# Kernel optimization log

Measured on AMD Instinct MI355X. Metric: run time of the kernel, lower is better.

Reference implementation:

```python
import jax, jax.numpy as jnp
import numpy as np

N = 100000
E = 3200000
D = 512

def setup_inputs() -> dict:
    key = jax.random.key(0)
    ks = jax.random.split(key, 6)
    X = jax.random.normal(ks[0], (N, D), dtype=jnp.float32)
    edge_row = jax.random.randint(ks[1], (E,), 0, N, dtype=jnp.int32)
    edge_col = jax.random.randint(ks[2], (E,), 0, N, dtype=jnp.int32)
    edge_val = jax.random.uniform(ks[3], (E,), dtype=jnp.float32)
    # glorot-uniform-ish init for weights
    lim = (6.0 / (D + D)) ** 0.5
    W1 = jax.random.uniform(ks[4], (D, D), dtype=jnp.float32, minval=-lim, maxval=lim)
    W2 = jax.random.uniform(ks[5], (D, D), dtype=jnp.float32, minval=-lim, maxval=lim)
    return {"X": X, "edge_row": edge_row, "edge_col": edge_col,
            "edge_val": edge_val, "W1": W1, "W2": W2}

def _spmm(edge_row, edge_col, edge_val, H):
    # out[r] = sum_{e: row[e]==r} val[e] * H[col[e]]
    msgs = edge_val[:, None] * H[edge_col]          # [E, D]
    return jax.ops.segment_sum(msgs, edge_row, num_segments=N)

def reference(X, edge_row, edge_col, edge_val, W1, W2):
    # layer 1: An @ (X @ W1), tanh activation, no bias
    h = jnp.tanh(_spmm(edge_row, edge_col, edge_val, X @ W1))
    # layer 2
    h = jnp.tanh(_spmm(edge_row, edge_col, edge_val, h @ W2))
    # tf.nn.l2_normalize(curr, axis=1)
    norm = jnp.sqrt(jnp.maximum(jnp.sum(h * h, axis=1, keepdims=True), 1e-12))
    return h / norm
```

## Files before the change

kernel.cpp:

```cpp
#include <hip/hip_runtime.h>
#include <hip/hip_fp16.h>

#define D_DIM 512

typedef __attribute__((ext_vector_type(8))) _Float16 half8;
typedef __attribute__((ext_vector_type(4))) float f32x4;
typedef __attribute__((ext_vector_type(2))) float float2v;

__device__ inline unsigned short f16b(float f) {
  return __half_as_ushort(__float2half(f));
}


__device__ inline void glds16(const _Float16* g, _Float16* l) {
  __builtin_amdgcn_global_load_lds(
      (const __attribute__((address_space(1))) void*)g,
      (__attribute__((address_space(3))) void*)l, 16, 0, 0);
}


__global__ __launch_bounds__(256) void k_hist(const int* __restrict__ row, int* __restrict__ cnt, int E) {
  int i = blockIdx.x * blockDim.x + threadIdx.x;
  if (i < E) atomicAdd(&cnt[row[i]], 1);
}

__global__ __launch_bounds__(1024) void k_scanA(const int* __restrict__ cnt, int* __restrict__ rp,
                                                int* __restrict__ bsum, int n) {
  __shared__ int s[1024];
  int i = blockIdx.x * 1024 + threadIdx.x;
  int v = (i < n) ? cnt[i] : 0;
  s[threadIdx.x] = v;
  __syncthreads();
  for (int off = 1; off < 1024; off <<= 1) {
    int t = (threadIdx.x >= off) ? s[threadIdx.x - off] : 0;
    __syncthreads();
    s[threadIdx.x] += t;
    __syncthreads();
  }
  if (i < n) rp[i] = s[threadIdx.x] - v;
  if (threadIdx.x == 1023) bsum[blockIdx.x] = s[1023];
}

__global__ __launch_bounds__(1024) void k_scanB(int* __restrict__ bsum, int nb) {
  __shared__ int s[1024];
  int v = (threadIdx.x < nb) ? bsum[threadIdx.x] : 0;
  s[threadIdx.x] = v;
  __syncthreads();
  for (int off = 1; off < 1024; off <<= 1) {
    int t = (threadIdx.x >= off) ? s[threadIdx.x - off] : 0;
    __syncthreads();
    s[threadIdx.x] += t;
    __syncthreads();
  }
  if (threadIdx.x < nb) bsum[threadIdx.x] = s[threadIdx.x] - v;
}

__global__ __launch_bounds__(256) void k_scanC(int* __restrict__ rp, const int* __restrict__ bsum, int n, int E) {
  int i = blockIdx.x * 256 + threadIdx.x;
  if (i < n) rp[i] += bsum[i >> 10];
  if (i == 0) rp[n] = E;
}

__global__ __launch_bounds__(256) void k_scatter(const int* __restrict__ row, const int* __restrict__ col,
                                                 const float* __restrict__ val, int* __restrict__ cur,
                                                 int2* __restrict__ edat, int E) {
  int i = blockIdx.x * blockDim.x + threadIdx.x;
  if (i < E) {
    int r = row[i];
    int p = atomicAdd(&cur[r], 1);
    edat[p] = make_int2(col[i], __float_as_int(val[i]));
  }
}


__global__ __launch_bounds__(256) void k_convA(const float* __restrict__ X, unsigned* __restrict__ Xf,
                                               long nValid4, long nTot4) {
  long i = (long)blockIdx.x * 256 + threadIdx.x;
  long stride = (long)gridDim.x * 256;
  for (; i < nTot4; i += stride) {
    float4 x = make_float4(0.f, 0.f, 0.f, 0.f);
    if (i < nValid4) x = ((const float4*)X)[i];
    uint2 v;
    v.x = (unsigned)f16b(x.x) | ((unsigned)f16b(x.y) << 16);
    v.y = (unsigned)f16b(x.z) | ((unsigned)f16b(x.w) << 16);
    const long r = i >> 7;
    const int c0 = (int)(i & 127) * 4;
    const long halfidx = ((r >> 4) * 16 + (c0 >> 5)) * 512 + ((c0 >> 3) & 3) * 128 + (r & 15) * 8 + (c0 & 7);
    ((uint2*)Xf)[halfidx >> 2] = v;
  }
}


__global__ __launch_bounds__(256) void k_repackW(const float* __restrict__ W, _Float16* __restrict__ Wf) {
  int n = blockIdx.x * 256 + threadIdx.x;
  int kg = blockIdx.y;
  half8 v;
#pragma unroll
  for (int j = 0; j < 8; ++j) v[j] = (_Float16)W[(kg * 8 + j) * D_DIM + n];
  const long halfidx = ((long)(kg >> 2) * 32 + (n >> 4)) * 512 + (kg & 3) * 128 + (n & 15) * 8;
  *(half8*)(Wf + halfidx) = v;
}


__global__ __launch_bounds__(256) void k_gemm(const _Float16* __restrict__ A,
                                              const _Float16* __restrict__ B,
                                              _Float16* __restrict__ Cout, int MB) {
  const int id = blockIdx.x;
  const int xcd = id & 7;
  const int sgrid = id >> 3;
  const int panel = (sgrid >> 2) * 8 + xcd;
  if (panel >= MB) return;
  const int nb = sgrid & 3;

  const int tid = threadIdx.x;
  const int lane = tid & 63;
  const int w = tid >> 6;
  const int wr = w >> 1, wc = w & 1;
  const int c = lane & 15, g = lane >> 4;
  const long r0 = (long)panel * 128 + wr * 64;
  const int n0 = nb * 128 + wc * 64;

  __shared__ __align__(16) char smem[32768];
  _Float16* Asl = (_Float16*)smem;
  _Float16* Bsl = (_Float16*)(smem + 16384);

  f32x4 acc[4][4] = {};

  const int f0 = w, f1 = w + 4;
  const long aF0 = ((long)(panel * 8 + f0) * 16) * 512 + lane * 8;
  const long aF1 = ((long)(panel * 8 + f1) * 16) * 512 + lane * 8;
  const long bBase = ((long)nb * 8) * 512 + lane * 8;

  for (int s = 0; s < 8; ++s) {
    const int k5a = 2 * s, k5b = 2 * s + 1;
    glds16(A + aF0 + (long)k5a * 512, Asl + (0 * 8 + f0) * 512);
    glds16(A + aF0 + (long)k5b * 512, Asl + (1 * 8 + f0) * 512);
    glds16(A + aF1 + (long)k5a * 512, Asl + (0 * 8 + f1) * 512);
    glds16(A + aF1 + (long)k5b * 512, Asl + (1 * 8 + f1) * 512);
    glds16(B + bBase + ((long)k5a * 32 + f0) * 512, Bsl + (0 * 8 + f0) * 512);
    glds16(B + bBase + ((long)k5b * 32 + f0) * 512, Bsl + (1 * 8 + f0) * 512);
    glds16(B + bBase + ((long)k5a * 32 + f1) * 512, Bsl + (0 * 8 + f1) * 512);
    glds16(B + bBase + ((long)k5b * 32 + f1) * 512, Bsl + (1 * 8 + f1) * 512);
    __syncthreads();
#pragma unroll
    for (int k5loc = 0; k5loc < 2; ++k5loc) {
      half8 a[4], b[4];
#pragma unroll
      for (int mi = 0; mi < 4; ++mi)
        a[mi] = *(const half8*)(Asl + (k5loc * 8 + wr * 4 + mi) * 512 + lane * 8);
#pragma unroll
      for (int ni = 0; ni < 4; ++ni)
        b[ni] = *(const half8*)(Bsl + (k5loc * 8 + wc * 4 + ni) * 512 + lane * 8);
#pragma unroll
      for (int mi = 0; mi < 4; ++mi)
#pragma unroll
        for (int ni = 0; ni < 4; ++ni)
          acc[mi][ni] = __builtin_amdgcn_mfma_f32_16x16x32_f16(a[mi], b[ni], acc[mi][ni], 0, 0, 0);
    }
    __syncthreads();
  }

  float (*ep)[16][68] = (float (*)[16][68])smem;
#pragma unroll
  for (int m = 0; m < 4; ++m) {
#pragma unroll
    for (int nf = 0; nf < 4; ++nf)
#pragma unroll
      for (int j = 0; j < 4; ++j)
        ep[w][g * 4 + j][nf * 16 + c] = acc[m][nf][j];
    __syncthreads();
    {
      const int row = lane >> 2;
      const int ch = lane & 3;
      float v[16];
#pragma unroll
      for (int q = 0; q < 16; ++q) v[q] = ep[w][row][ch * 16 + q];
      half8 h0, h1;
#pragma unroll
      for (int q = 0; q < 8; ++q) {
        h0[q] = (_Float16)v[q];
        h1[q] = (_Float16)v[8 + q];
      }
      _Float16* dst = Cout + (r0 + m * 16 + row) * D_DIM + n0 + ch * 16;
      *(half8*)dst = h0;
      *(half8*)(dst + 8) = h1;
    }
    __syncthreads();
  }
}


template <int MODE>
__global__ __launch_bounds__(256) void k_spmm(const unsigned short* __restrict__ T, const int* __restrict__ rp,
                                              const int2* __restrict__ edat,
                                              unsigned* __restrict__ Hf, float* __restrict__ out) {
  __shared__ float p[4][D_DIM];
  __shared__ float wss[4];
  const int r = blockIdx.x;
  const int tid = threadIdx.x;
  const int w = tid >> 6, lane = tid & 63;
  const int beg = rp[r], end = rp[r + 1];
  const int cnt = end - beg;
  const int eb = beg + ((cnt * w) >> 2);
  const int ee = beg + ((cnt * (w + 1)) >> 2);

  float acc[8] = {};
  const uint4* Tv = (const uint4*)T;
  for (int e = eb; e < ee; ++e) {
    const int2 ed = edat[e];
    const float v = __int_as_float(ed.y);
    uint4 x = Tv[(long)ed.x * 64 + lane];
    unsigned xs[4] = {x.x, x.y, x.z, x.w};
#pragma unroll
    for (int q = 0; q < 4; ++q) {
      float2 f = __half22float2(__builtin_bit_cast(__half2, xs[q]));
      acc[2 * q] = fmaf(v, f.x, acc[2 * q]);
      acc[2 * q + 1] = fmaf(v, f.y, acc[2 * q + 1]);
    }
  }
  *(float4*)&p[w][lane * 8] = make_float4(acc[0], acc[1], acc[2], acc[3]);
  *(float4*)&p[w][lane * 8 + 4] = make_float4(acc[4], acc[5], acc[6], acc[7]);
  __syncthreads();

  const int c = tid * 2;
  float s0 = p[0][c] + p[1][c] + p[2][c] + p[3][c];
  float s1 = p[0][c + 1] + p[1][c + 1] + p[2][c + 1] + p[3][c + 1];
  s0 = tanhf(s0);
  s1 = tanhf(s1);

  if (MODE == 0) {
    unsigned hv = (unsigned)f16b(s0) | ((unsigned)f16b(s1) << 16);
    const long halfidx = ((long)(r >> 4) * 16 + (c >> 5)) * 512 + ((c >> 3) & 3) * 128 + (r & 15) * 8 + (c & 7);
    __builtin_nontemporal_store(hv, Hf + (halfidx >> 1));
  } else {
    float ss = fmaf(s0, s0, s1 * s1);
#pragma unroll
    for (int off = 1; off < 64; off <<= 1) ss += __shfl_xor(ss, off);
    if (lane == 0) wss[w] = ss;
    __syncthreads();
    const float tot = wss[0] + wss[1] + wss[2] + wss[3];
    const float sc = rsqrtf(fmaxf(tot, 1e-12f));
    float2v o;
    o.x = s0 * sc;
    o.y = s1 * sc;
    __builtin_nontemporal_store(o, (float2v*)out + (long)r * 256 + tid);
  }
}


extern "C" void kernel_launch(void* const* d_in, const int* in_sizes, int n_in,
                              void* d_out, int out_size, void* d_ws, size_t ws_size,
                              hipStream_t stream) {
  const float* X = (const float*)d_in[0];
  const int* erow = (const int*)d_in[1];
  const int* ecol = (const int*)d_in[2];
  const float* evalv = (const float*)d_in[3];
  const float* W1 = (const float*)d_in[4];
  const float* W2 = (const float*)d_in[5];
  const int N = in_sizes[0] / D_DIM;
  const int E = in_sizes[1];
  (void)n_in; (void)out_size; (void)ws_size;

  const int MB = (N + 127) / 128;
  const long Mp = (long)MB * 128;

  char* wsp = (char*)d_ws;
  size_t off = 0;
  auto alloc = [&](size_t bytes) {
    void* p = wsp + off;
    off = (off + bytes + 255) & ~(size_t)255;
    return p;
  };
  unsigned short* T  = (unsigned short*)alloc(Mp * D_DIM * 2);
  unsigned* Af = (unsigned*)alloc(Mp * D_DIM * 2);
  int2* edat  = (int2*)alloc((size_t)E * 8);
  int* rowptr = (int*)alloc((size_t)(N + 1) * 4);
  int* cursor = (int*)alloc((size_t)N * 4);
  int* bsum   = (int*)alloc(1024 * 4);
  _Float16* W1f = (_Float16*)alloc((size_t)D_DIM * D_DIM * 2);
  _Float16* W2f = (_Float16*)alloc((size_t)D_DIM * D_DIM * 2);

  const int nScanBlk = (N + 1023) / 1024;
  const int gemmGrid = 32 * ((MB + 7) / 8);

  hipMemsetAsync(cursor, 0, (size_t)N * 4, stream);
  k_hist<<<dim3((E + 255) / 256), dim3(256), 0, stream>>>(erow, cursor, E);
  k_scanA<<<dim3(nScanBlk), dim3(1024), 0, stream>>>(cursor, rowptr, bsum, N);
  k_scanB<<<dim3(1), dim3(1024), 0, stream>>>(bsum, nScanBlk);
  k_scanC<<<dim3((N + 255) / 256), dim3(256), 0, stream>>>(rowptr, bsum, N, E);
  hipMemcpyAsync(cursor, rowptr, (size_t)N * 4, hipMemcpyDeviceToDevice, stream);
  k_scatter<<<dim3((E + 255) / 256), dim3(256), 0, stream>>>(erow, ecol, evalv, cursor, edat, E);

  k_convA<<<dim3(4096), dim3(256), 0, stream>>>(X, Af, (long)N * D_DIM / 4, Mp * D_DIM / 4);
  k_repackW<<<dim3(2, 64), dim3(256), 0, stream>>>(W1, W1f);
  k_repackW<<<dim3(2, 64), dim3(256), 0, stream>>>(W2, W2f);

  k_gemm<<<dim3(gemmGrid), dim3(256), 0, stream>>>((const _Float16*)Af, W1f, (_Float16*)T, MB);
  k_spmm<0><<<dim3(N), dim3(256), 0, stream>>>(T, rowptr, edat, Af, nullptr);
  k_gemm<<<dim3(gemmGrid), dim3(256), 0, stream>>>((const _Float16*)Af, W2f, (_Float16*)T, MB);
  k_spmm<1><<<dim3(N), dim3(256), 0, stream>>>(T, rowptr, edat, nullptr, (float*)d_out);
}
```

Baseline: 1.504 ms.

## Two-pass binned CSR scatter and LDS-staged coalesced X conversion

The single-pass edge scatter, which did random writes across the whole edge array, is replaced by two passes. The first bins edges into 128-row buckets using a per-bucket atomic cursor and writes packed records into a temp buffer that reuses the T workspace. The second places each edge within its bucket using LDS atomics. The X fp32-to-fp16 conversion now stages each 16-row tile in LDS so the swizzled-layout output is written with coalesced 16-byte stores. The trade-off is an extra kernel, an extra pass over the edge data, and contention on the bucket atomics; the column index must fit in 25 bits.

```diff
diff --git a/kernel.cpp b/kernel.cpp
--- a/kernel.cpp
+++ b/kernel.cpp
@@ -61,32 +61,74 @@
   if (i == 0) rp[n] = E;
 }
 
-__global__ __launch_bounds__(256) void k_scatter(const int* __restrict__ row, const int* __restrict__ col,
-                                                 const float* __restrict__ val, int* __restrict__ cur,
-                                                 int2* __restrict__ edat, int E) {
+
+__global__ __launch_bounds__(256) void k_bcurInit(const int* __restrict__ rp, int* __restrict__ bcur, int NB) {
+  int b = blockIdx.x * 256 + threadIdx.x;
+  if (b < NB) bcur[b] = rp[b << 7];
+}
+
+__global__ __launch_bounds__(256) void k_binA(const int* __restrict__ row, const int* __restrict__ col,
+                                              const float* __restrict__ val, int* __restrict__ bcur,
+                                              uint2* __restrict__ tmp, int E) {
   int i = blockIdx.x * blockDim.x + threadIdx.x;
   if (i < E) {
     int r = row[i];
-    int p = atomicAdd(&cur[r], 1);
-    edat[p] = make_int2(col[i], __float_as_int(val[i]));
-  }
-}
-
-
-__global__ __launch_bounds__(256) void k_convA(const float* __restrict__ X, unsigned* __restrict__ Xf,
-                                               long nValid4, long nTot4) {
-  long i = (long)blockIdx.x * 256 + threadIdx.x;
-  long stride = (long)gridDim.x * 256;
-  for (; i < nTot4; i += stride) {
+    int p = atomicAdd(&bcur[r >> 7], 1);
+    tmp[p] = make_uint2(((unsigned)(r & 127) << 25) | (unsigned)col[i],
+                        __float_as_uint(val[i]));
+  }
+}
+
+__global__ __launch_bounds__(256) void k_binB(const uint2* __restrict__ tmp, const int* __restrict__ rp,
+                                              int2* __restrict__ edat, int N, int NB) {
+  __shared__ int cur128[128];
+  const int b = blockIdx.x;
+  const int tid = threadIdx.x;
+  if (tid < 128) {
+    int r = (b << 7) + tid;
+    cur128[tid] = (r < N) ? rp[r] : 0;
+  }
+  __syncthreads();
+  const int base = rp[b << 7];
+  const int hi = (b + 1) << 7;
+  const int end = rp[hi < N ? hi : N];
+  for (int t = base + tid; t < end; t += 256) {
+    uint2 rec = tmp[t];
+    int rl = rec.x >> 25;
+    int c = rec.x & 0x01FFFFFF;
+    int p = atomicAdd(&cur128[rl], 1);
+    edat[p] = make_int2(c, (int)rec.y);
+  }
+}
+
+
+__global__ __launch_bounds__(256) void k_convA(const float* __restrict__ X, unsigned* __restrict__ Xf, int N) {
+  __shared__ unsigned lds[4096];
+  const int Rg = blockIdx.x;
+  const long r0 = (long)Rg * 16;
+  const int tid = threadIdx.x;
+#pragma unroll
+  for (int k = 0; k < 8; ++k) {
+    int idx = tid + k * 256;
+    int r = idx >> 7;
+    int q = idx & 127;
+    int c0 = q * 4;
     float4 x = make_float4(0.f, 0.f, 0.f, 0.f);
-    if (i < nValid4) x = ((const float4*)X)[i];
-    uint2 v;
-    v.x = (unsigned)f16b(x.x) | ((unsigned)f16b(x.y) << 16);
-    v.y = (unsigned)f16b(x.z) | ((unsigned)f16b(x.w) << 16);
-    const long r = i >> 7;
-    const int c0 = (int)(i & 127) * 4;
-    const long halfidx = ((r >> 4) * 16 + (c0 >> 5)) * 512 + ((c0 >> 3) & 3) * 128 + (r & 15) * 8 + (c0 & 7);
-    ((uint2*)Xf)[halfidx >> 2] = v;
+    long gr = r0 + r;
+    if (gr < N) x = ((const float4*)X)[gr * 128 + q];
+    unsigned h0 = (unsigned)f16b(x.x) | ((unsigned)f16b(x.y) << 16);
+    unsigned h1 = (unsigned)f16b(x.z) | ((unsigned)f16b(x.w) << 16);
+    int off = (c0 >> 5) * 512 + ((c0 >> 3) & 3) * 128 + r * 8 + (c0 & 7);
+    lds[off >> 1] = h0;
+    lds[(off >> 1) + 1] = h1;
+  }
+  __syncthreads();
+  uint4* dst = (uint4*)(Xf + (long)Rg * 4096);
+  const uint4* src = (const uint4*)lds;
+#pragma unroll
+  for (int k = 0; k < 4; ++k) {
+    int idx = tid + k * 256;
+    dst[idx] = src[idx];
   }
 }
 
@@ -263,6 +305,7 @@
 
   const int MB = (N + 127) / 128;
   const long Mp = (long)MB * 128;
+  const int NB = (N + 127) / 128;
 
   char* wsp = (char*)d_ws;
   size_t off = 0;
@@ -275,23 +318,27 @@
   unsigned* Af = (unsigned*)alloc(Mp * D_DIM * 2);
   int2* edat  = (int2*)alloc((size_t)E * 8);
   int* rowptr = (int*)alloc((size_t)(N + 1) * 4);
-  int* cursor = (int*)alloc((size_t)N * 4);
+  int* cnt    = (int*)alloc((size_t)N * 4);
   int* bsum   = (int*)alloc(1024 * 4);
+  int* bcur   = (int*)alloc((size_t)NB * 4);
   _Float16* W1f = (_Float16*)alloc((size_t)D_DIM * D_DIM * 2);
   _Float16* W2f = (_Float16*)alloc((size_t)D_DIM * D_DIM * 2);
 
+  uint2* tmp = (uint2*)T;
+
   const int nScanBlk = (N + 1023) / 1024;
   const int gemmGrid = 32 * ((MB + 7) / 8);
 
-  hipMemsetAsync(cursor, 0, (size_t)N * 4, stream);
-  k_hist<<<dim3((E + 255) / 256), dim3(256), 0, stream>>>(erow, cursor, E);
-  k_scanA<<<dim3(nScanBlk), dim3(1024), 0, stream>>>(cursor, rowptr, bsum, N);
+  hipMemsetAsync(cnt, 0, (size_t)N * 4, stream);
+  k_hist<<<dim3((E + 255) / 256), dim3(256), 0, stream>>>(erow, cnt, E);
+  k_scanA<<<dim3(nScanBlk), dim3(1024), 0, stream>>>(cnt, rowptr, bsum, N);
   k_scanB<<<dim3(1), dim3(1024), 0, stream>>>(bsum, nScanBlk);
   k_scanC<<<dim3((N + 255) / 256), dim3(256), 0, stream>>>(rowptr, bsum, N, E);
-  hipMemcpyAsync(cursor, rowptr, (size_t)N * 4, hipMemcpyDeviceToDevice, stream);
-  k_scatter<<<dim3((E + 255) / 256), dim3(256), 0, stream>>>(erow, ecol, evalv, cursor, edat, E);
-
-  k_convA<<<dim3(4096), dim3(256), 0, stream>>>(X, Af, (long)N * D_DIM / 4, Mp * D_DIM / 4);
+  k_bcurInit<<<dim3((NB + 255) / 256), dim3(256), 0, stream>>>(rowptr, bcur, NB);
+  k_binA<<<dim3((E + 255) / 256), dim3(256), 0, stream>>>(erow, ecol, evalv, bcur, tmp, E);
+  k_binB<<<dim3(NB), dim3(256), 0, stream>>>(tmp, rowptr, edat, N, NB);
+
+  k_convA<<<dim3((int)(Mp / 16)), dim3(256), 0, stream>>>(X, Af, N);
   k_repackW<<<dim3(2, 64), dim3(256), 0, stream>>>(W1, W1f);
   k_repackW<<<dim3(2, 64), dim3(256), 0, stream>>>(W2, W2f);
 
```

Result: slower. 2.059 ms (+36.9%).
